# Kernel optimization log

Measured on AMD Instinct MI355X. Metric: run time of the kernel, lower is better.

## Reference

```python
import jax, jax.numpy as jnp
import numpy as np
import itertools

N_OBJECTS = 6  # subsets of range(6), sizes 1..6 -> 63 subsets

def _subset_groups():
    # group subsets by length so each group runs as one batched LSTM
    groups = {}
    for m in range(1, N_OBJECTS + 1):
        for s in itertools.combinations(range(6), m):
            groups.setdefault(m, []).append(list(s))
    return [(m, np.asarray(v, dtype=np.int32)) for m, v in groups.items()]

SUBSET_GROUPS = _subset_groups()


def _lstm_final_h(x, W_ih, W_hh, b_ih, b_hh):
    """x: [B,T,D] -> final hidden state [B,H]. PyTorch gate order i,f,g,o."""
    H = W_hh.shape[1]
    B = x.shape[0]
    # precompute input projections for all timesteps: [B,T,4H]
    xz = jnp.einsum('btd,gd->btg', x, W_ih) + b_ih + b_hh

    def step(carry, xt):
        h, c = carry
        z = xt + h @ W_hh.T
        i, f, g, o = jnp.split(z, 4, axis=-1)
        c = jax.nn.sigmoid(f) * c + jax.nn.sigmoid(i) * jnp.tanh(g)
        h = jax.nn.sigmoid(o) * jnp.tanh(c)
        return (h, c), None

    h0 = jnp.zeros((B, H), x.dtype)
    (h, _), _ = jax.lax.scan(step, (h0, h0), jnp.swapaxes(xz, 0, 1))
    return h


def setup_inputs() -> dict:
    key = jax.random.key(0)
    ks = jax.random.split(key, 10)
    D, H, FC, A = 16, 128, 256, 10
    mb = 8192
    s = lambda k, shape, fan: jax.random.normal(k, shape, jnp.float32) * (1.0 / np.sqrt(fan))
    return {
        'x_input': jax.random.normal(ks[0], (mb, 6, D), jnp.float32),
        'W_ih': s(ks[1], (4 * H, D), D),
        'W_hh': s(ks[2], (4 * H, H), H),
        'b_ih': jnp.zeros((4 * H,), jnp.float32),
        'b_hh': jnp.zeros((4 * H,), jnp.float32),
        'fc1_W': s(ks[3], (FC, H), H),
        'fc1_b': jnp.zeros((FC,), jnp.float32),
        'fc2_W': s(ks[4], (A, FC), FC),
        'fc2_b': jnp.zeros((A,), jnp.float32),
    }


def reference(x_input, W_ih, W_hh, b_ih, b_hh, fc1_W, fc1_b, fc2_W, fc2_b):
    mb = x_input.shape[0]
    H = W_hh.shape[1]
    hs = []
    # subsets of the same length are batched into one LSTM pass (fused form of
    # the original 63-iteration python loop); aggregation is permutation-invariant
    for m, idx in SUBSET_GROUPS:
        nL = idx.shape[0]
        xg = x_input[:, idx, :]                       # [mb, nL, m, D] gather
        xg = xg.reshape(mb * nL, m, x_input.shape[-1])
        h = _lstm_final_h(xg, W_ih, W_hh, b_ih, b_hh)  # [mb*nL, H]
        hs.append(h.reshape(mb, nL, H))
    holder = jnp.concatenate(hs, axis=1)              # [mb, 63, H]
    x = jnp.max(holder, axis=1)                       # aggregate == 'max'
    x = jax.nn.relu(x @ fc1_W.T + fc1_b)
    x = x @ fc2_W.T + fc2_b
    return jax.nn.log_softmax(x, axis=-1)
```

## Files before the change

### kernel.cpp

```cpp
#include <hip/hip_runtime.h>
#include <hip/hip_bf16.h>

#define BLOCK   512
#define NSAMP   16
#define HDIM    128
#define DDIM    16
#define NOBJ    6
#define NSLOT   17

typedef __attribute__((ext_vector_type(8))) short bf16x8;
typedef __attribute__((ext_vector_type(4))) float f32x4;

constexpr int pc6(int m)  { int c = 0; for (int i = 0; i < 6; ++i) c += (m >> i) & 1; return c; }
constexpr int msb6(int m) { int b = -1; for (int i = 0; i < 6; ++i) if (m & (1 << i)) b = i; return b; }

struct GChild { int jo, sl; bool bar; };
struct Plan3 {
    int    gps [32];
    int    gbeg[33];
    GChild ch  [63];
    int    lvlG[8];
    bool   ok;
};
constexpr Plan3 make_plan3() {
    Plan3 P{};
    P.ok = true;
    int  slotOf[64] = {};
    bool busy[NSLOT] = {};
    int  pendingFree[NSLOT] = {};
    int  npend = 0;
    int  g = 0, cidx = 0;
    for (int d = 1; d <= 6; ++d) {
        P.lvlG[d] = g;
        for (int Pm = 0; Pm < 64; ++Pm) {
            if (pc6(Pm) != d - 1) continue;
            if (Pm != 0 && msb6(Pm) == 5) continue;
            P.gps[g]  = (Pm == 0) ? -1 : slotOf[Pm];
            P.gbeg[g] = cidx;
            if (Pm != 0) pendingFree[npend++] = slotOf[Pm];
            const int j0 = (Pm == 0) ? 0 : msb6(Pm) + 1;
            for (int j = j0; j <= 5; ++j) {
                const int M = Pm | (1 << j);
                P.ch[cidx].jo  = j;
                P.ch[cidx].bar = false;
                int sl = -1;
                if (j < 5) {
                    int fs = -1;
                    for (int s = 0; s < NSLOT; ++s) if (!busy[s]) { fs = s; break; }
                    if (fs < 0) {
                        P.ch[cidx].bar = true;
                        for (int i = 0; i < npend; ++i) busy[pendingFree[i]] = false;
                        npend = 0;
                        for (int s = 0; s < NSLOT; ++s) if (!busy[s]) { fs = s; break; }
                        if (fs < 0) P.ok = false;
                    }
                    if (fs >= 0) { busy[fs] = true; slotOf[M] = fs; sl = fs; }
                }
                P.ch[cidx].sl = sl;
                ++cidx;
            }
            ++g;
        }
        for (int i = 0; i < npend; ++i) busy[pendingFree[i]] = false;
        npend = 0;
    }
    P.lvlG[7] = g;
    P.gbeg[g] = cidx;
    if (g != 32 || cidx != 63) P.ok = false;
    return P;
}
constexpr Plan3 PL3 = make_plan3();
static_assert(PL3.ok, "plan allocation failed");
static_assert(PL3.lvlG[7] == 32, "32 groups expected");
static_assert(PL3.gbeg[32] == 63, "63 children expected");

#define LOG2E   1.44269504f
#define TWOL2E  2.88539008f
#define SLOT_SH 2048

__device__ __forceinline__ unsigned short f2bf(float x) {
    union { float f; unsigned int u; } a; a.f = x;
    unsigned int r = (a.u + 0x7FFFu + ((a.u >> 16) & 1u)) >> 16;
    return (unsigned short)r;
}
__device__ __forceinline__ unsigned pk2(float a, float b) {
    union { __hip_bfloat162 h; unsigned u; } z;
    z.h = __float22bfloat162_rn(float2{a, b});
    return z.u;
}
__device__ __forceinline__ float bflo(unsigned p) {
    union { unsigned u; float f; } a; a.u = p << 16; return a.f;
}
__device__ __forceinline__ float bfhi(unsigned p) {
    union { unsigned u; float f; } a; a.u = p & 0xFFFF0000u; return a.f;
}


__global__ __launch_bounds__(BLOCK)
__attribute__((amdgpu_waves_per_eu(2, 4)))
void subset_lstm_skew_kernel(
    const float* __restrict__ x_input,
    const float* __restrict__ W_ih,
    const float* __restrict__ W_hh,
    const float* __restrict__ b_ih,
    const float* __restrict__ b_hh,
    const float* __restrict__ fc1_W,
    const float* __restrict__ fc1_b,
    const float* __restrict__ fc2_W,
    const float* __restrict__ fc2_b,
    float* __restrict__ out)
{
    __shared__ __align__(16) unsigned short hs [NSLOT * SLOT_SH];
    __shared__ __align__(16) unsigned short csb[NSLOT * SLOT_SH];
    __shared__ __align__(16) unsigned short xb[NOBJ * 4 * NSAMP * 8];
    float* s_maxh  = (float*)hs;
    float* s_fc1   = (float*)(hs + 4096);
    float* s_logit = (float*)xb;

    const int t      = threadIdx.x;
    const int w      = t >> 6;
    const int lane   = t & 63;
    const int quad   = lane >> 4;
    const int m16    = lane & 15;
    const int s_base = blockIdx.x * NSAMP;

    for (int idx = t; idx < NOBJ * 4 * NSAMP * 8; idx += BLOCK) {
        const int j = idx & 7, n = (idx >> 3) & 15, q = (idx >> 7) & 3, obj = idx >> 9;
        float v;
        if (q < 2) v = x_input[(s_base + n) * (NOBJ * DDIM) + obj * DDIM + q * 8 + j];
        else       v = (q == 2 && j == 0) ? 1.0f : 0.0f;
        xb[idx] = f2bf(v);
    }

    bf16x8 wf[4][5];
    #pragma unroll
    for (int g = 0; g < 4; ++g) {
        const float sc = (g == 2) ? TWOL2E : -LOG2E;
        const int grow = g * HDIM + w * 16 + m16;
        const float* whr = W_hh + grow * HDIM;
        const float* wir = W_ih + grow * DDIM;
        #pragma unroll
        for (int q = 0; q < 4; ++q) {
            union { unsigned short u[8]; bf16x8 v; } pk;
            #pragma unroll
            for (int j = 0; j < 8; ++j)
                pk.u[j] = f2bf(sc * whr[q * 32 + quad * 8 + j]);
            wf[g][q] = pk.v;
        }
        {
            union { unsigned short u[8]; bf16x8 v; } pk;
            #pragma unroll
            for (int j = 0; j < 8; ++j) {
                float v = 0.0f;
                if (quad < 2) v = sc * wir[quad * 8 + j];
                else if (quad == 2 && j == 0) v = sc * (b_ih[grow] + b_hh[grow]);
                pk.u[j] = f2bf(v);
            }
            wf[g][4] = pk.v;
        }
    }

    float mh[4] = {-1e30f, -1e30f, -1e30f, -1e30f};
    const int kslot = w * 2 + (quad >> 1);
    unsigned short* const c_lane = &csb[(((w * 4 + quad) * NSAMP) + m16) * 4];

    auto pointwise_node = [&](const f32x4 (&acc)[4], uint2 cpk, int sl) {
        float cn4[4], hn4[4];
        #pragma unroll
        for (int r = 0; r < 4; ++r) {
            const unsigned p = (r < 2) ? cpk.x : cpk.y;
            const float cprev = (r & 1) ? bfhi(p) : bflo(p);
            const float u  = 1.0f + __builtin_amdgcn_exp2f(acc[0][r]);
            const float q  = 1.0f + __builtin_amdgcn_exp2f(acc[1][r]);
            const float v  = 1.0f + __builtin_amdgcn_exp2f(acc[2][r]);
            const float qo = 1.0f + __builtin_amdgcn_exp2f(acc[3][r]);
            const float uv  = u * v;
            const float num = fmaf(q, v - 2.0f, cprev * uv);
            const float cn  = num * __builtin_amdgcn_rcpf(q * uv);
            const float wt  = 1.0f + __builtin_amdgcn_exp2f(TWOL2E * cn);
            const float h   = (wt - 2.0f) * __builtin_amdgcn_rcpf(qo * wt);
            cn4[r] = cn; hn4[r] = h;
            mh[r] = fmaxf(mh[r], h);
        }
        if (sl >= 0) {
            uint2 cw; cw.x = pk2(cn4[0], cn4[1]); cw.y = pk2(cn4[2], cn4[3]);
            *(uint2*)(c_lane + sl * SLOT_SH) = cw;
            uint2 hw; hw.x = pk2(hn4[0], hn4[1]); hw.y = pk2(hn4[2], hn4[3]);
            *(uint2*)&hs[((sl * 16 + kslot) * NSAMP + m16) * 8 + (quad & 1) * 4] = hw;
        }
    };

    #pragma unroll
    for (int d = 1; d <= 6; ++d) {
        __syncthreads();
        const int gBeg = PL3.lvlG[d];
        const int gEnd = PL3.lvlG[d + 1];
        #pragma unroll
        for (int gi = gBeg; gi < gEnd; ++gi) {
            const int ps = PL3.gps[gi];
            f32x4 zh[4];
            uint2 cpkP; cpkP.x = 0u; cpkP.y = 0u;
            #pragma unroll
            for (int g2 = 0; g2 < 4; ++g2) zh[g2] = f32x4{0.f, 0.f, 0.f, 0.f};
            if (ps >= 0) {
                cpkP = *(const uint2*)(c_lane + ps * SLOT_SH);
                #pragma unroll
                for (int q = 0; q < 4; ++q) {
                    const bf16x8 bh = *(const bf16x8*)
                        &hs[((ps * 16 + q * 4 + quad) * NSAMP + m16) * 8];
                    #pragma unroll
                    for (int g2 = 0; g2 < 4; ++g2)
                        zh[g2] = __builtin_amdgcn_mfma_f32_16x16x32_bf16(
                            wf[g2][q], bh, zh[g2], 0, 0, 0);
                }
            }
            #pragma unroll
            for (int ci = PL3.gbeg[gi]; ci < PL3.gbeg[gi + 1]; ++ci) {
                if (PL3.ch[ci].bar) __syncthreads();
                const bf16x8 bfx = *(const bf16x8*)
                    &xb[((PL3.ch[ci].jo * 4 + quad) * NSAMP + m16) * 8];
                f32x4 acc[4];
                #pragma unroll
                for (int g2 = 0; g2 < 4; ++g2)
                    acc[g2] = __builtin_amdgcn_mfma_f32_16x16x32_bf16(
                        wf[g2][4], bfx, zh[g2], 0, 0, 0);
                pointwise_node(acc, cpkP, PL3.ch[ci].sl);
            }
        }
    }

    __syncthreads();
    {
        float4 v; v.x = mh[0]; v.y = mh[1]; v.z = mh[2]; v.w = mh[3];
        *(float4*)&s_maxh[m16 * HDIM + w * 16 + quad * 4] = v;
    }
    __syncthreads();

    {
        const int f  = t & 255;
        const int sh = t >> 8;
        float a1[8];
        #pragma unroll
        for (int s = 0; s < 8; ++s) a1[s] = fc1_b[f];
        for (int k4 = 0; k4 < HDIM / 4; ++k4) {
            const float4 wv = *(const float4*)&fc1_W[f * HDIM + k4 * 4];
            #pragma unroll
            for (int s = 0; s < 8; ++s) {
                const float4 h4 = *(const float4*)&s_maxh[(sh * 8 + s) * HDIM + k4 * 4];
                a1[s] += wv.x * h4.x + wv.y * h4.y + wv.z * h4.z + wv.w * h4.w;
            }
        }
        #pragma unroll
        for (int s = 0; s < 8; ++s)
            s_fc1[(sh * 8 + s) * 256 + f] = fmaxf(a1[s], 0.0f);
    }
    __syncthreads();

    if (t < NSAMP * 10) {
        const int s = t / 10, a = t % 10;
        float acc2 = fc2_b[a];
        for (int f4 = 0; f4 < 256 / 4; ++f4) {
            const float4 wv = *(const float4*)&fc2_W[a * 256 + f4 * 4];
            const float4 v  = *(const float4*)&s_fc1[s * 256 + f4 * 4];
            acc2 += wv.x * v.x + wv.y * v.y + wv.z * v.z + wv.w * v.w;
        }
        s_logit[s * 10 + a] = acc2;
    }
    __syncthreads();

    if (t < NSAMP) {
        float m = -1e30f;
        #pragma unroll
        for (int a = 0; a < 10; ++a) m = fmaxf(m, s_logit[t * 10 + a]);
        float sum = 0.0f;
        #pragma unroll
        for (int a = 0; a < 10; ++a) sum += __expf(s_logit[t * 10 + a] - m);
        const float lse = m + __logf(sum);
        #pragma unroll
        for (int a = 0; a < 10; ++a)
            out[(s_base + t) * 10 + a] = s_logit[t * 10 + a] - lse;
    }
}

extern "C" void kernel_launch(void* const* d_in, const int* in_sizes, int n_in,
                              void* d_out, int out_size, void* d_ws, size_t ws_size,
                              hipStream_t stream)
{
    (void)d_ws; (void)ws_size; (void)n_in; (void)out_size;

    const float* x   = (const float*)d_in[0];
    const float* Wih = (const float*)d_in[1];
    const float* Whh = (const float*)d_in[2];
    const float* bih = (const float*)d_in[3];
    const float* bhh = (const float*)d_in[4];
    const float* f1w = (const float*)d_in[5];
    const float* f1b = (const float*)d_in[6];
    const float* f2w = (const float*)d_in[7];
    const float* f2b = (const float*)d_in[8];

    const int mb = in_sizes[0] / (NOBJ * DDIM);
    dim3 grid(mb / NSAMP), block(BLOCK);
    subset_lstm_skew_kernel<<<grid, block, 0, stream>>>(
        x, Wih, Whh, bih, bhh, f1w, f1b, f2w, f2b, (float*)d_out);
}
```

Before: 190.8 us.

## Replace fully unrolled subset tree with table-driven loop and fewer LDS slots

The compile-time-unrolled traversal of the 63 subset nodes becomes a single rolled loop driven by packed control words, which are built at compile time and copied into LDS. Each word holds the object index, the slot, the barrier flags and the parent slot. The slot count drops from 17 to 14, which cuts LDS use per block and may allow more resident blocks. In exchange each node pays scalar decode and branch overhead, and the compiler can no longer schedule across node boundaries. Extra barriers may also be needed when slots run out.

```diff
diff --git a/kernel.cpp b/kernel.cpp
--- a/kernel.cpp
+++ b/kernel.cpp
@@ -6,7 +6,7 @@
 #define HDIM    128
 #define DDIM    16
 #define NOBJ    6
-#define NSLOT   17
+#define NSLOT   14
 
 typedef __attribute__((ext_vector_type(8))) short bf16x8;
 typedef __attribute__((ext_vector_type(4))) float f32x4;
@@ -49,6 +49,7 @@
                     for (int s = 0; s < NSLOT; ++s) if (!busy[s]) { fs = s; break; }
                     if (fs < 0) {
                         P.ch[cidx].bar = true;
+                        if (npend == 0) P.ok = false;
                         for (int i = 0; i < npend; ++i) busy[pendingFree[i]] = false;
                         npend = 0;
                         for (int s = 0; s < NSLOT; ++s) if (!busy[s]) { fs = s; break; }
@@ -73,6 +74,28 @@
 static_assert(PL3.ok, "plan allocation failed");
 static_assert(PL3.lvlG[7] == 32, "32 groups expected");
 static_assert(PL3.gbeg[32] == 63, "63 children expected");
+
+struct CWords { unsigned w[64]; };
+constexpr CWords make_cwords() {
+    CWords C{};
+    for (int i = 0; i < 64; ++i) C.w[i] = 0;
+    for (int g = 0; g < 32; ++g) {
+        const int cB = PL3.gbeg[g], cE = PL3.gbeg[g + 1];
+        for (int ci = cB; ci < cE; ++ci) {
+            const unsigned jo = (unsigned)PL3.ch[ci].jo;
+            const unsigned sl = PL3.ch[ci].sl < 0 ? 31u : (unsigned)PL3.ch[ci].sl;
+            const unsigned rb = PL3.ch[ci].bar ? 1u : 0u;
+            const unsigned ng = (ci == cB) ? 1u : 0u;
+            const unsigned ps = PL3.gps[g] < 0 ? 31u : (unsigned)PL3.gps[g];
+            C.w[ci] = jo | (sl << 3) | (rb << 8) | (ng << 9) | (ps << 10);
+        }
+    }
+    for (int d = 1; d <= 6; ++d)
+        C.w[PL3.gbeg[PL3.lvlG[d]]] |= (1u << 15);
+    C.w[63] = 0;
+    return C;
+}
+__device__ const CWords d_cw = make_cwords();
 
 #define LOG2E   1.44269504f
 #define TWOL2E  2.88539008f
@@ -113,6 +136,7 @@
     __shared__ __align__(16) unsigned short hs [NSLOT * SLOT_SH];
     __shared__ __align__(16) unsigned short csb[NSLOT * SLOT_SH];
     __shared__ __align__(16) unsigned short xb[NOBJ * 4 * NSAMP * 8];
+    __shared__ unsigned cw_lds[64];
     float* s_maxh  = (float*)hs;
     float* s_fc1   = (float*)(hs + 4096);
     float* s_logit = (float*)xb;
@@ -123,6 +147,8 @@
     const int quad   = lane >> 4;
     const int m16    = lane & 15;
     const int s_base = blockIdx.x * NSAMP;
+
+    if (t < 64) cw_lds[t] = d_cw.w[t];
 
     for (int idx = t; idx < NOBJ * 4 * NSAMP * 8; idx += BLOCK) {
         const int j = idx & 7, n = (idx >> 3) & 15, q = (idx >> 7) & 3, obj = idx >> 9;
@@ -160,73 +186,80 @@
         }
     }
 
+    __syncthreads();
+
     float mh[4] = {-1e30f, -1e30f, -1e30f, -1e30f};
     const int kslot = w * 2 + (quad >> 1);
-    unsigned short* const c_lane = &csb[(((w * 4 + quad) * NSAMP) + m16) * 4];
-
-    auto pointwise_node = [&](const f32x4 (&acc)[4], uint2 cpk, int sl) {
+    unsigned short* const c_lane = &csb[t * 4];
+    unsigned short* const h_rd   = &hs[quad * (NSAMP * 8) + m16 * 8];
+    unsigned short* const h_wr   = &hs[kslot * (NSAMP * 8) + m16 * 8 + (quad & 1) * 4];
+
+    f32x4 zh[4];
+    float cp4[4];
+    #pragma unroll
+    for (int g2 = 0; g2 < 4; ++g2) zh[g2] = f32x4{0.f, 0.f, 0.f, 0.f};
+    #pragma unroll
+    for (int r = 0; r < 4; ++r) cp4[r] = 0.0f;
+
+    unsigned cw = __builtin_amdgcn_readfirstlane(cw_lds[0]);
+
+    #pragma unroll 1
+    for (int ci = 0; ci < 63; ++ci) {
+        const unsigned cw_n = cw_lds[ci + 1];
+        if (cw & (1u << 15)) __syncthreads();
+        if (cw & (1u << 9)) {
+            const int ps = (cw >> 10) & 31;
+            #pragma unroll
+            for (int g2 = 0; g2 < 4; ++g2) zh[g2] = f32x4{0.f, 0.f, 0.f, 0.f};
+            if (ps != 31) {
+                const uint2 cpk = *(const uint2*)(c_lane + (ps << 11));
+                cp4[0] = bflo(cpk.x); cp4[1] = bfhi(cpk.x);
+                cp4[2] = bflo(cpk.y); cp4[3] = bfhi(cpk.y);
+                const unsigned short* hb = h_rd + (ps << 11);
+                #pragma unroll
+                for (int q = 0; q < 4; ++q) {
+                    const bf16x8 bh = *(const bf16x8*)(hb + q * 512);
+                    #pragma unroll
+                    for (int g2 = 0; g2 < 4; ++g2)
+                        zh[g2] = __builtin_amdgcn_mfma_f32_16x16x32_bf16(
+                            wf[g2][q], bh, zh[g2], 0, 0, 0);
+                }
+            } else {
+                #pragma unroll
+                for (int r = 0; r < 4; ++r) cp4[r] = 0.0f;
+            }
+        }
+        if (cw & (1u << 8)) __syncthreads();
+        const int jo = cw & 7;
+        const int sl = (cw >> 3) & 31;
+        const bf16x8 bfx = *(const bf16x8*)&xb[((jo * 4 + quad) * NSAMP + m16) * 8];
+        f32x4 acc[4];
+        #pragma unroll
+        for (int g2 = 0; g2 < 4; ++g2)
+            acc[g2] = __builtin_amdgcn_mfma_f32_16x16x32_bf16(
+                wf[g2][4], bfx, zh[g2], 0, 0, 0);
         float cn4[4], hn4[4];
         #pragma unroll
         for (int r = 0; r < 4; ++r) {
-            const unsigned p = (r < 2) ? cpk.x : cpk.y;
-            const float cprev = (r & 1) ? bfhi(p) : bflo(p);
             const float u  = 1.0f + __builtin_amdgcn_exp2f(acc[0][r]);
             const float q  = 1.0f + __builtin_amdgcn_exp2f(acc[1][r]);
             const float v  = 1.0f + __builtin_amdgcn_exp2f(acc[2][r]);
             const float qo = 1.0f + __builtin_amdgcn_exp2f(acc[3][r]);
             const float uv  = u * v;
-            const float num = fmaf(q, v - 2.0f, cprev * uv);
+            const float num = fmaf(q, v - 2.0f, cp4[r] * uv);
             const float cn  = num * __builtin_amdgcn_rcpf(q * uv);
             const float wt  = 1.0f + __builtin_amdgcn_exp2f(TWOL2E * cn);
             const float h   = (wt - 2.0f) * __builtin_amdgcn_rcpf(qo * wt);
             cn4[r] = cn; hn4[r] = h;
             mh[r] = fmaxf(mh[r], h);
         }
-        if (sl >= 0) {
-            uint2 cw; cw.x = pk2(cn4[0], cn4[1]); cw.y = pk2(cn4[2], cn4[3]);
-            *(uint2*)(c_lane + sl * SLOT_SH) = cw;
+        if (sl != 31) {
+            uint2 cw2; cw2.x = pk2(cn4[0], cn4[1]); cw2.y = pk2(cn4[2], cn4[3]);
+            *(uint2*)(c_lane + (sl << 11)) = cw2;
             uint2 hw; hw.x = pk2(hn4[0], hn4[1]); hw.y = pk2(hn4[2], hn4[3]);
-            *(uint2*)&hs[((sl * 16 + kslot) * NSAMP + m16) * 8 + (quad & 1) * 4] = hw;
-        }
-    };
-
-    #pragma unroll
-    for (int d = 1; d <= 6; ++d) {
-        __syncthreads();
-        const int gBeg = PL3.lvlG[d];
-        const int gEnd = PL3.lvlG[d + 1];
-        #pragma unroll
-        for (int gi = gBeg; gi < gEnd; ++gi) {
-            const int ps = PL3.gps[gi];
-            f32x4 zh[4];
-            uint2 cpkP; cpkP.x = 0u; cpkP.y = 0u;
-            #pragma unroll
-            for (int g2 = 0; g2 < 4; ++g2) zh[g2] = f32x4{0.f, 0.f, 0.f, 0.f};
-            if (ps >= 0) {
-                cpkP = *(const uint2*)(c_lane + ps * SLOT_SH);
-                #pragma unroll
-                for (int q = 0; q < 4; ++q) {
-                    const bf16x8 bh = *(const bf16x8*)
-                        &hs[((ps * 16 + q * 4 + quad) * NSAMP + m16) * 8];
-                    #pragma unroll
-                    for (int g2 = 0; g2 < 4; ++g2)
-                        zh[g2] = __builtin_amdgcn_mfma_f32_16x16x32_bf16(
-                            wf[g2][q], bh, zh[g2], 0, 0, 0);
-                }
-            }
-            #pragma unroll
-            for (int ci = PL3.gbeg[gi]; ci < PL3.gbeg[gi + 1]; ++ci) {
-                if (PL3.ch[ci].bar) __syncthreads();
-                const bf16x8 bfx = *(const bf16x8*)
-                    &xb[((PL3.ch[ci].jo * 4 + quad) * NSAMP + m16) * 8];
-                f32x4 acc[4];
-                #pragma unroll
-                for (int g2 = 0; g2 < 4; ++g2)
-                    acc[g2] = __builtin_amdgcn_mfma_f32_16x16x32_bf16(
-                        wf[g2][4], bfx, zh[g2], 0, 0, 0);
-                pointwise_node(acc, cpkP, PL3.ch[ci].sl);
-            }
-        }
+            *(uint2*)(h_wr + (sl << 11)) = hw;
+        }
+        cw = __builtin_amdgcn_readfirstlane(cw_n);
     }
 
     __syncthreads();
```

Result: slower. 212.5 us (+11.4%).

## Keep cell state in registers and enlarge slot pool to remove recycle barriers

Applied to the files above, without the earlier changes.

Raises the hidden-state slot count so the compile-time plan needs no mid-level recycle barriers, and asserts that none remain. The cell-state scratch in LDS is dropped: each lane keeps its packed bf16 cell state in a register array indexed by compile-time slot, and the object-5 input fragment is loaded once and reused. The aim is fewer __syncthreads and less LDS traffic. In exchange the hidden-state buffer in LDS grows and per-thread register use rises, which could lower occupancy or cause spills.

```diff
diff --git a/kernel.cpp b/kernel.cpp
--- a/kernel.cpp
+++ b/kernel.cpp
@@ -6,7 +6,7 @@
 #define HDIM    128
 #define DDIM    16
 #define NOBJ    6
-#define NSLOT   17
+#define NSLOT   20
 
 typedef __attribute__((ext_vector_type(8))) short bf16x8;
 typedef __attribute__((ext_vector_type(4))) float f32x4;
@@ -49,6 +49,7 @@
                     for (int s = 0; s < NSLOT; ++s) if (!busy[s]) { fs = s; break; }
                     if (fs < 0) {
                         P.ch[cidx].bar = true;
+                        if (npend == 0) P.ok = false;
                         for (int i = 0; i < npend; ++i) busy[pendingFree[i]] = false;
                         npend = 0;
                         for (int s = 0; s < NSLOT; ++s) if (!busy[s]) { fs = s; break; }
@@ -73,6 +74,12 @@
 static_assert(PL3.ok, "plan allocation failed");
 static_assert(PL3.lvlG[7] == 32, "32 groups expected");
 static_assert(PL3.gbeg[32] == 63, "63 children expected");
+constexpr int count_bars() {
+    int n = 0;
+    for (int i = 0; i < 63; ++i) if (PL3.ch[i].bar) ++n;
+    return n;
+}
+static_assert(count_bars() == 0, "NSLOT=20 must eliminate all recycle barriers");
 
 #define LOG2E   1.44269504f
 #define TWOL2E  2.88539008f
@@ -111,7 +118,6 @@
     float* __restrict__ out)
 {
     __shared__ __align__(16) unsigned short hs [NSLOT * SLOT_SH];
-    __shared__ __align__(16) unsigned short csb[NSLOT * SLOT_SH];
     __shared__ __align__(16) unsigned short xb[NOBJ * 4 * NSAMP * 8];
     float* s_maxh  = (float*)hs;
     float* s_fc1   = (float*)(hs + 4096);
@@ -160,22 +166,23 @@
         }
     }
 
+    __syncthreads();
+    const bf16x8 bfx5 = *(const bf16x8*)&xb[((5 * 4 + quad) * NSAMP + m16) * 8];
+
     float mh[4] = {-1e30f, -1e30f, -1e30f, -1e30f};
     const int kslot = w * 2 + (quad >> 1);
-    unsigned short* const c_lane = &csb[(((w * 4 + quad) * NSAMP) + m16) * 4];
-
-    auto pointwise_node = [&](const f32x4 (&acc)[4], uint2 cpk, int sl) {
+    uint2 c_pk[NSLOT];
+
+    auto pw_tail = [&](const f32x4 (&acc)[4], const float (&cp4)[4], int sl) {
         float cn4[4], hn4[4];
         #pragma unroll
         for (int r = 0; r < 4; ++r) {
-            const unsigned p = (r < 2) ? cpk.x : cpk.y;
-            const float cprev = (r & 1) ? bfhi(p) : bflo(p);
             const float u  = 1.0f + __builtin_amdgcn_exp2f(acc[0][r]);
             const float q  = 1.0f + __builtin_amdgcn_exp2f(acc[1][r]);
             const float v  = 1.0f + __builtin_amdgcn_exp2f(acc[2][r]);
             const float qo = 1.0f + __builtin_amdgcn_exp2f(acc[3][r]);
             const float uv  = u * v;
-            const float num = fmaf(q, v - 2.0f, cprev * uv);
+            const float num = fmaf(q, v - 2.0f, cp4[r] * uv);
             const float cn  = num * __builtin_amdgcn_rcpf(q * uv);
             const float wt  = 1.0f + __builtin_amdgcn_exp2f(TWOL2E * cn);
             const float h   = (wt - 2.0f) * __builtin_amdgcn_rcpf(qo * wt);
@@ -183,8 +190,8 @@
             mh[r] = fmaxf(mh[r], h);
         }
         if (sl >= 0) {
-            uint2 cw; cw.x = pk2(cn4[0], cn4[1]); cw.y = pk2(cn4[2], cn4[3]);
-            *(uint2*)(c_lane + sl * SLOT_SH) = cw;
+            c_pk[sl].x = pk2(cn4[0], cn4[1]);
+            c_pk[sl].y = pk2(cn4[2], cn4[3]);
             uint2 hw; hw.x = pk2(hn4[0], hn4[1]); hw.y = pk2(hn4[2], hn4[3]);
             *(uint2*)&hs[((sl * 16 + kslot) * NSAMP + m16) * 8 + (quad & 1) * 4] = hw;
         }
@@ -199,11 +206,12 @@
         for (int gi = gBeg; gi < gEnd; ++gi) {
             const int ps = PL3.gps[gi];
             f32x4 zh[4];
-            uint2 cpkP; cpkP.x = 0u; cpkP.y = 0u;
+            float cp4[4];
             #pragma unroll
             for (int g2 = 0; g2 < 4; ++g2) zh[g2] = f32x4{0.f, 0.f, 0.f, 0.f};
             if (ps >= 0) {
-                cpkP = *(const uint2*)(c_lane + ps * SLOT_SH);
+                cp4[0] = bflo(c_pk[ps].x); cp4[1] = bfhi(c_pk[ps].x);
+                cp4[2] = bflo(c_pk[ps].y); cp4[3] = bfhi(c_pk[ps].y);
                 #pragma unroll
                 for (int q = 0; q < 4; ++q) {
                     const bf16x8 bh = *(const bf16x8*)
@@ -213,18 +221,21 @@
                         zh[g2] = __builtin_amdgcn_mfma_f32_16x16x32_bf16(
                             wf[g2][q], bh, zh[g2], 0, 0, 0);
                 }
+            } else {
+                #pragma unroll
+                for (int r = 0; r < 4; ++r) cp4[r] = 0.0f;
             }
             #pragma unroll
             for (int ci = PL3.gbeg[gi]; ci < PL3.gbeg[gi + 1]; ++ci) {
-                if (PL3.ch[ci].bar) __syncthreads();
-                const bf16x8 bfx = *(const bf16x8*)
-                    &xb[((PL3.ch[ci].jo * 4 + quad) * NSAMP + m16) * 8];
+                const int jo = PL3.ch[ci].jo;
+                const bf16x8 bfx = (jo == 5) ? bfx5 :
+                    *(const bf16x8*)&xb[((jo * 4 + quad) * NSAMP + m16) * 8];
                 f32x4 acc[4];
                 #pragma unroll
                 for (int g2 = 0; g2 < 4; ++g2)
                     acc[g2] = __builtin_amdgcn_mfma_f32_16x16x32_bf16(
                         wf[g2][4], bfx, zh[g2], 0, 0, 0);
-                pointwise_node(acc, cpkP, PL3.ch[ci].sl);
+                pw_tail(acc, cp4, PL3.ch[ci].sl);
             }
         }
     }
```

Result: no change. 191.0 us (+0.1%).
